# Kernel tuning notes

Hardware: AMD Instinct MI355X
Metric: run time of the kernel (lower is better)

## Reference

```python
import jax, jax.numpy as jnp
import numpy as np
import math

TOPK = 13
NUM_CLASSES = 80
ALPHA = 1.0
BETA = 6.0
EPS = 1e-9


def _ciou(box1, box2, eps=1e-7):
    # box1: (b, n, 1, 4) gt xyxy, box2: (b, 1, A, 4) pred xyxy -> (b, n, A)
    b1x1, b1y1, b1x2, b1y2 = [box1[..., i] for i in range(4)]
    b2x1, b2y1, b2x2, b2y2 = [box2[..., i] for i in range(4)]
    w1, h1 = b1x2 - b1x1, b1y2 - b1y1
    w2, h2 = b2x2 - b2x1, b2y2 - b2y1
    inter = jnp.clip(jnp.minimum(b1x2, b2x2) - jnp.maximum(b1x1, b2x1), 0.0) * \
            jnp.clip(jnp.minimum(b1y2, b2y2) - jnp.maximum(b1y1, b2y1), 0.0)
    union = w1 * h1 + w2 * h2 - inter + eps
    iou = inter / union
    cw = jnp.maximum(b1x2, b2x2) - jnp.minimum(b1x1, b2x1)
    ch = jnp.maximum(b1y2, b2y2) - jnp.minimum(b1y1, b2y1)
    c2 = cw * cw + ch * ch + eps
    rho2 = ((b2x1 + b2x2 - b1x1 - b1x2) ** 2 + (b2y1 + b2y2 - b1y1 - b1y2) ** 2) / 4.0
    v = (4.0 / math.pi ** 2) * (jnp.arctan(w2 / (h2 + eps)) - jnp.arctan(w1 / (h1 + eps))) ** 2
    alpha = jax.lax.stop_gradient(v / (v - iou + (1.0 + eps)))
    return iou - (rho2 / c2 + v * alpha)


def _assign(pd_scores, pd_bboxes, anc_points, gt_labels, gt_probs, gt_bboxes, mask_gt):
    b, A, C = pd_scores.shape
    n = gt_bboxes.shape[1]
    bidx = jnp.arange(b)
    labels = gt_labels.reshape(b, n).astype(jnp.int32)

    # --- get_box_metrics ---
    bbox_scores = pd_scores[bidx[:, None], :, labels]                      # (b, n, A)
    overlaps = jnp.clip(_ciou(gt_bboxes[:, :, None, :], pd_bboxes[:, None, :, :]), 0.0)
    align_metric = bbox_scores ** ALPHA * overlaps ** BETA                 # (b, n, A)

    # --- select_candidates_in_gts ---
    lt, rb = gt_bboxes[..., :2], gt_bboxes[..., 2:]
    deltas = jnp.concatenate([anc_points[None, None] - lt[:, :, None],
                              rb[:, :, None] - anc_points[None, None]], axis=-1)
    mask_in_gts = (deltas.min(-1) > EPS).astype(pd_scores.dtype)           # (b, n, A)

    # --- select_topk_candidates ---
    metrics = align_metric * mask_in_gts
    _, topk_idxs = jax.lax.top_k(metrics, TOPK)
    topk_mask = jnp.broadcast_to(mask_gt.astype(bool), (b, n, TOPK))
    topk_idxs = jnp.where(topk_mask, topk_idxs, 0)
    cnt = jnp.zeros((b, n, A), jnp.int32).at[
        bidx[:, None, None], jnp.arange(n)[None, :, None], topk_idxs].add(1)
    is_in_topk = jnp.where(cnt > 1, 0, cnt).astype(metrics.dtype)
    mask_pos = is_in_topk * mask_in_gts * mask_gt                          # (b, n, A)

    # --- select_highest_overlaps ---
    tgt = (jnp.arange(n)[None, :, None] * mask_pos).astype(jnp.int32)
    max_mask = overlaps == overlaps.max(axis=1, keepdims=True)
    tgt = tgt * max_mask.astype(jnp.int32)                                 # (b, n, A)
    unique_bbox_idx = tgt.argmax(1)                                        # (b, A)
    fg_mask = mask_pos.sum(-2)                                             # (b, A)

    # --- get_targets ---
    tgt_flat = tgt + (bidx * n)[:, None, None]                             # (b, n, A)
    target_labels = labels.reshape(-1)[tgt_flat]                           # (b, n, A)
    sel = jnp.take_along_axis(tgt_flat, unique_bbox_idx[:, None, :], axis=1)[:, 0]
    target_bboxes = gt_bboxes.reshape(-1, 4)[sel]                          # (b, A, 4)

    # hard targets: per-anchor class histogram over gt axis, corrected
    hard = jnp.zeros((b, A, C), jnp.int32).at[
        bidx[:, None, None], jnp.arange(A)[None, None, :], target_labels].add(1)
    fg_columns = hard.sum(1).argmax(1)                                     # (b,)
    diff = (n - fg_mask).astype(jnp.int32)                                 # (b, A)
    col_mask = jax.nn.one_hot(fg_columns, C, dtype=jnp.int32)[:, None, :]  # (b, 1, C)
    non_fg_count = (hard * (1 - col_mask)).sum(-1)                         # (b, A)
    hard = hard - diff[..., None] * col_mask
    denom = (fg_mask - non_fg_count)[..., None] * col_mask                 # (b, A, C) float
    safe = jnp.where(denom != 0, denom, 1.0)
    hard = jnp.where(denom != 0, jnp.trunc(hard / safe).astype(jnp.int32), hard)
    hard = jnp.clip(hard, 0, 1)  # multilabel (>1) clamped to 1, negatives to 0

    # --- normalization of target scores ---
    pos_align = (align_metric * mask_pos).max(-1, keepdims=True)           # (b, n, 1)
    pos_overlaps = (overlaps * mask_pos).max(-1, keepdims=True)
    norm = (align_metric * pos_overlaps * mask_pos / (pos_align + EPS)).max(-2)[..., None]  # (b, A, 1)
    target_scores = hard.astype(pd_scores.dtype) * norm                    # (b, A, C)
    return target_bboxes, target_scores, fg_mask.astype(bool), tgt


def setup_inputs() -> dict:
    key = jax.random.key(0)
    ks = jax.random.split(key, 8)
    B, N, C = 32, 32, 80
    # YOLO anchor-point grid for 640x640, strides 8/16/32 -> A = 8400
    pts = []
    for s, g in ((8, 80), (16, 40), (32, 20)):
        c = (jnp.arange(g, dtype=jnp.float32) + 0.5) * s
        yy, xx = jnp.meshgrid(c, c, indexing="ij")
        pts.append(jnp.stack([xx.ravel(), yy.ravel()], -1))
    anc_points = jnp.concatenate(pts, 0)
    A = anc_points.shape[0]
    pd_scores = jax.random.uniform(ks[0], (B, A, C), jnp.float32)
    pcxy = anc_points[None] + 20.0 * jax.random.normal(ks[1], (B, A, 2), jnp.float32)
    pwh = jax.random.uniform(ks[2], (B, A, 2), jnp.float32, minval=10.0, maxval=120.0)
    pd_bboxes = jnp.concatenate([pcxy - pwh / 2, pcxy + pwh / 2], -1)
    gcxy = jax.random.uniform(ks[3], (B, N, 2), jnp.float32, minval=60.0, maxval=580.0)
    gwh = jax.random.uniform(ks[4], (B, N, 2), jnp.float32, minval=10.0, maxval=120.0)
    gt_bboxes = jnp.concatenate([gcxy - gwh / 2, gcxy + gwh / 2], -1)
    gt_labels = jax.random.randint(ks[5], (B, N, 1), 0, C).astype(jnp.int32)
    gt_probs = jax.random.uniform(ks[6], (B, N, 1), jnp.float32)
    n_valid = jax.random.randint(ks[7], (B, 1, 1), 1, N + 1)
    mask_gt = (jnp.arange(N)[None, :, None] < n_valid).astype(jnp.float32)
    return {"pd_scores": pd_scores, "pd_bboxes": pd_bboxes, "anc_points": anc_points,
            "gt_labels": gt_labels, "gt_probs": gt_probs, "gt_bboxes": gt_bboxes,
            "mask_gt": mask_gt}


def reference(pd_scores, pd_bboxes, anc_points, gt_labels, gt_probs, gt_bboxes, mask_gt):
    return _assign(pd_scores, pd_bboxes, anc_points, gt_labels, gt_probs, gt_bboxes, mask_gt)
```

## Files before the change

kernel.cpp:

```cpp
#include <hip/hip_runtime.h>
#include <math.h>

#define BB 32
#define NN 32
#define AA 8400
#define CC 80
#define TK 13
#define CAND 512
#define MAXP (NN*TK)

__device__ int      g_ccnt[BB*NN];
__device__ int      g_cand[BB*NN*CAND];
__device__ unsigned g_posmask[BB*AA];
__device__ float    g_posalign[BB*NN];
__device__ float    g_posov[BB*NN];
__device__ int      g_pcnt[BB];
__device__ int      g_plist[BB*MAXP];

struct PdPre { float x1,y1,x2,y2, area, sx, sy, at; };

__device__ __forceinline__ float ciou_j(const PdPre& q, float4 g, float garea,
                                        float gsx, float gsy, float gatan) {
  float iw = fmaxf(fminf(q.x2, g.z) - fmaxf(q.x1, g.x), 0.0f);
  float ih = fmaxf(fminf(q.y2, g.w) - fmaxf(q.y1, g.y), 0.0f);
  float inter = iw * ih;
  float uni = q.area + garea - inter + 1e-7f;
  float iou = inter / uni;
  float cw = fmaxf(q.x2, g.z) - fminf(q.x1, g.x);
  float ch = fmaxf(q.y2, g.w) - fminf(q.y1, g.y);
  float c2 = cw*cw + ch*ch + 1e-7f;
  float dx = gsx - q.sx, dy = gsy - q.sy;
  float rho2 = (dx*dx + dy*dy) * 0.25f;
  float dat = gatan - q.at;
  float v = (float)(4.0/(M_PI*M_PI)) * dat * dat;
  float alpha = v / (v - iou + (1.0f + 1e-7f));
  return fmaxf(iou - (rho2/c2 + v*alpha), 0.0f);
}

__device__ __forceinline__ PdPre pd_prep(float4 p) {
  PdPre q;
  float w1 = p.z - p.x, h1 = p.w - p.y;
  q.x1 = p.x; q.y1 = p.y; q.x2 = p.z; q.y2 = p.w;
  q.area = w1*h1; q.sx = p.x + p.z; q.sy = p.y + p.w;
  q.at = atanf(w1 / (h1 + 1e-7f));
  return q;
}

__global__ __launch_bounds__(256) void kfill(const float* __restrict__ gt_bboxes,
                                             float* __restrict__ out_bbox,
                                             float* __restrict__ out_scores,
                                             float* __restrict__ out_fg,
                                             float* __restrict__ out_tgt) {
  const size_t NS4 = (size_t)BB*AA*CC/4;
  const size_t NT4 = (size_t)BB*NN*AA/4;
  const size_t NF4 = (size_t)BB*AA/4;
  const size_t NP4 = (size_t)BB*AA/4;
  const size_t NB4 = (size_t)BB*AA;
  const size_t total = NS4 + NT4 + NF4 + NP4 + NB4;
  float4 z4 = make_float4(0.f,0.f,0.f,0.f);
  for (size_t i = (size_t)blockIdx.x*256 + threadIdx.x; i < total;
       i += (size_t)gridDim.x*256) {
    if (i < NS4) ((float4*)out_scores)[i] = z4;
    else if (i < NS4+NT4) ((float4*)out_tgt)[i-NS4] = z4;
    else if (i < NS4+NT4+NF4) ((float4*)out_fg)[i-NS4-NT4] = z4;
    else if (i < NS4+NT4+NF4+NP4) ((float4*)g_posmask)[i-NS4-NT4-NF4] = z4;
    else {
      size_t k = i - NS4 - NT4 - NF4 - NP4;
      int b = (int)(k / AA);
      ((float4*)out_bbox)[k] = *(const float4*)&gt_bboxes[b*NN*4];
    }
  }
  size_t gid = (size_t)blockIdx.x*256 + threadIdx.x;
  if (gid < BB*NN) g_ccnt[gid] = 0;
  if (gid < BB) g_pcnt[gid] = 0;
}

__global__ __launch_bounds__(256) void kA(const float* __restrict__ anc,
                                          const float* __restrict__ gt_bboxes,
                                          const float* __restrict__ mask_gt) {
  int b = blockIdx.y, t = threadIdx.x;
  int a = blockIdx.x*256 + t;
  __shared__ __align__(16) float4 gbox[NN];
  __shared__ int smask[NN];
  if (t < NN) {
    gbox[t] = *(const float4*)&gt_bboxes[(b*NN + t)*4];
    smask[t] = (mask_gt[b*NN + t] != 0.0f) ? 1 : 0;
  }
  __syncthreads();
  if (a >= AA) return;
  float2 an = ((const float2*)anc)[a];
  #pragma unroll
  for (int j = 0; j < NN; ++j) {
    if (!smask[j]) continue;
    float4 g = gbox[j];
    float mn = fminf(fminf(an.x - g.x, an.y - g.y), fminf(g.z - an.x, g.w - an.y));
    if (mn > 1e-9f) {
      int s = atomicAdd(&g_ccnt[b*NN + j], 1);
      if (s < CAND) g_cand[(size_t)(b*NN + j)*CAND + s] = a;
    }
  }
}

__global__ __launch_bounds__(64) void k2(const float* __restrict__ mask_gt,
                                         const float* __restrict__ pd_scores,
                                         const float* __restrict__ pd_bboxes,
                                         const float* __restrict__ anc,
                                         const int* __restrict__ gt_labels,
                                         const float* __restrict__ gt_bboxes) {
  int bj = blockIdx.x;
  int b = bj >> 5, j = bj & 31;
  int lane = threadIdx.x;
  bool valid = (mask_gt[bj] != 0.0f);
  if (!valid) {
    if (lane == 0) { g_posalign[bj] = 0.0f; g_posov[bj] = 0.0f; }
    return;
  }
  int cnt = g_ccnt[bj]; if (cnt > CAND) cnt = CAND;
  int labj = gt_labels[bj];
  float4 g = *(const float4*)&gt_bboxes[bj*4];
  float w2 = g.z - g.x, h2 = g.w - g.y;
  float garea = w2*h2, gsx = g.x + g.z, gsy = g.y + g.w;
  float gatan = atanf(w2 / (h2 + 1e-7f));
  const float2* anc2 = (const float2*)anc;

  unsigned long long tk[TK];
  #pragma unroll
  for (int i = 0; i < TK; ++i) tk[i] = 0ull;
  auto ins = [&](unsigned long long key) {
    if (key > tk[TK-1]) {
      tk[TK-1] = key;
      #pragma unroll
      for (int i = TK-1; i > 0; --i) {
        if (tk[i] > tk[i-1]) {
          unsigned long long tmp = tk[i-1]; tk[i-1] = tk[i]; tk[i] = tmp;
        }
      }
    }
  };
  for (int c = lane; c < cnt; c += 64) {
    int a = g_cand[(size_t)bj*CAND + c];
    float4 p = *(const float4*)&pd_bboxes[(size_t)(b*AA + a)*4];
    float sc = pd_scores[(size_t)(b*AA + a)*CC + labj];
    PdPre q = pd_prep(p);
    float ov = ciou_j(q, g, garea, gsx, gsy, gatan);
    float ov2 = ov*ov;
    float metric = sc * (ov2*ov2*ov2);
    ins(((unsigned long long)__float_as_uint(metric) << 32)
        | (unsigned long long)(0xFFFFFFFFu - (unsigned)a));
  }
  if (lane < TK) {
    float2 an = anc2[lane];
    float mn = fminf(fminf(an.x - g.x, an.y - g.y), fminf(g.z - an.x, g.w - an.y));
    if (!(mn > 1e-9f))
      ins((unsigned long long)(0xFFFFFFFFu - (unsigned)lane));
  }
  unsigned long long myk = 0ull;
  for (int r = 0; r < TK; ++r) {
    unsigned long long m = tk[0];
    #pragma unroll
    for (int o = 32; o > 0; o >>= 1) {
      unsigned long long other = __shfl_xor(m, o, 64);
      if (other > m) m = other;
    }
    if (tk[0] == m) {
      #pragma unroll
      for (int i = 0; i < TK-1; ++i) tk[i] = tk[i+1];
      tk[TK-1] = 0ull;
    }
    if (lane == r) myk = m;
  }
  float pa = 0.0f, po = 0.0f;
  if (lane < TK && myk != 0ull) {
    unsigned a = 0xFFFFFFFFu - (unsigned)(myk & 0xFFFFFFFFull);
    float val = __uint_as_float((unsigned)(myk >> 32));
    float2 an = anc2[a];
    float mn = fminf(fminf(an.x - g.x, an.y - g.y), fminf(g.z - an.x, g.w - an.y));
    if (mn > 1e-9f) {
      unsigned old = atomicOr(&g_posmask[b*AA + a], 1u << j);
      if (old == 0u) {
        int idx = atomicAdd(&g_pcnt[b], 1);
        g_plist[b*MAXP + idx] = (int)a;
      }
      float4 p = *(const float4*)&pd_bboxes[(size_t)(b*AA + a)*4];
      PdPre q = pd_prep(p);
      float ov = ciou_j(q, g, garea, gsx, gsy, gatan);
      pa = val; po = ov;
    }
  }
  #pragma unroll
  for (int o = 32; o > 0; o >>= 1) {
    pa = fmaxf(pa, __shfl_xor(pa, o, 64));
    po = fmaxf(po, __shfl_xor(po, o, 64));
  }
  if (lane == 0) { g_posalign[bj] = pa; g_posov[bj] = po; }
}

__global__ __launch_bounds__(256) void k3(const float* __restrict__ pd_scores,
                                          const float* __restrict__ pd_bboxes,
                                          const float* __restrict__ gt_bboxes,
                                          const int* __restrict__ gt_labels,
                                          float* __restrict__ out_bbox,
                                          float* __restrict__ out_fg,
                                          float* __restrict__ out_tgt,
                                          float* __restrict__ out_scores) {
  int b = blockIdx.y, t = threadIdx.x;
  __shared__ __align__(16) float4 gbox[NN];
  __shared__ float garea[NN], gsx[NN], gsy[NN], gatan[NN], pal[NN], pov[NN];
  __shared__ int lab[NN];
  if (t < NN) {
    float4 g = *(const float4*)&gt_bboxes[(b*NN + t)*4];
    gbox[t] = g;
    float w2 = g.z - g.x, h2 = g.w - g.y;
    gsx[t] = g.x + g.z; gsy[t] = g.y + g.w;
    garea[t] = w2*h2;
    gatan[t] = atanf(w2 / (h2 + 1e-7f));
    lab[t] = gt_labels[b*NN + t];
    pal[t] = g_posalign[b*NN + t];
    pov[t] = g_posov[b*NN + t];
  }
  __syncthreads();
  int npos = g_pcnt[b];
  int si = blockIdx.x*8 + (t >> 5);
  if (si >= npos) return;
  int j = t & 31;
  int a = g_plist[b*MAXP + si];
  unsigned pm = g_posmask[b*AA + a];
  float4 p = *(const float4*)&pd_bboxes[(size_t)(b*AA + a)*4];
  PdPre q = pd_prep(p);
  float ovj = ciou_j(q, gbox[j], garea[j], gsx[j], gsy[j], gatan[j]);
  float maxo = ovj;
  #pragma unroll
  for (int o = 16; o > 0; o >>= 1) maxo = fmaxf(maxo, __shfl_xor(maxo, o, 64));
  bool pmj = (pm >> j) & 1u;
  bool tb = pmj && (ovj == maxo) && (j > 0);
  unsigned long long bal = __ballot(tb);
  unsigned tm = (t & 32) ? (unsigned)(bal >> 32) : (unsigned)(bal & 0xffffffffull);
  float contrib = 0.0f;
  if (pmj) {
    float sc = pd_scores[(size_t)(b*AA + a)*CC + lab[j]];
    float ov2 = ovj*ovj;
    float al = sc * (ov2*ov2*ov2);
    contrib = al * pov[j] / (pal[j] + 1e-9f);
  }
  float nrm = contrib;
  #pragma unroll
  for (int o = 16; o > 0; o >>= 1) nrm = fmaxf(nrm, __shfl_xor(nrm, o, 64));
  if (tb) out_tgt[(size_t)(b*NN + j)*AA + a] = (float)j;
  int fg = __popc(pm);
  int F = lab[0];
  unsigned m0 = 0u, m1 = 0u, m2 = 0u;
  int z = NN - __popc(tm);
  int cntF = z;
  {
    int l0 = lab[0];
    if (l0 < 32) m0 |= 1u << l0; else if (l0 < 64) m1 |= 1u << (l0-32); else m2 |= 1u << (l0-64);
  }
  unsigned tmp = tm;
  while (tmp) {
    int jj = __ffs(tmp) - 1; tmp &= tmp - 1;
    int l = lab[jj];
    if (l < 32) m0 |= 1u << l; else if (l < 64) m1 |= 1u << (l-32); else m2 |= 1u << (l-64);
    cntF += (l == F) ? 1 : 0;
  }
  bool hFv = (cntF + fg) != NN;
  size_t base = (size_t)(b*AA + a)*CC;
  {
    int c = j;
    bool bit = (m0 >> j) & 1u;
    bool ind = (c == F) ? hFv : bit;
    out_scores[base + c] = ind ? nrm : 0.0f;
  }
  {
    int c = j + 32;
    bool bit = (m1 >> j) & 1u;
    bool ind = (c == F) ? hFv : bit;
    out_scores[base + c] = ind ? nrm : 0.0f;
  }
  if (j < 16) {
    int c = j + 64;
    bool bit = (m2 >> j) & 1u;
    bool ind = (c == F) ? hFv : bit;
    out_scores[base + c] = ind ? nrm : 0.0f;
  }
  if (j == 0) {
    out_fg[b*AA + a] = 1.0f;
    int jmax = tm ? (31 - __clz(tm)) : 0;
    *(float4*)&out_bbox[(size_t)(b*AA + a)*4] = gbox[jmax];
  }
}

extern "C" void kernel_launch(void* const* d_in, const int* in_sizes, int n_in,
                              void* d_out, int out_size, void* d_ws, size_t ws_size,
                              hipStream_t stream) {
  const float* pd_scores = (const float*)d_in[0];
  const float* pd_bboxes = (const float*)d_in[1];
  const float* anc       = (const float*)d_in[2];
  const int*   gt_labels = (const int*)d_in[3];
  const float* gt_bboxes = (const float*)d_in[5];
  const float* mask_gt   = (const float*)d_in[6];

  float* out_bbox   = (float*)d_out;
  float* out_scores = out_bbox + (size_t)BB*AA*4;
  float* out_fg     = out_scores + (size_t)BB*AA*CC;
  float* out_tgt    = out_fg + (size_t)BB*AA;

  kfill<<<2048, 256, 0, stream>>>(gt_bboxes, out_bbox, out_scores, out_fg, out_tgt);
  dim3 ga((AA + 255)/256, BB);
  kA<<<ga, 256, 0, stream>>>(anc, gt_bboxes, mask_gt);
  k2<<<BB*NN, 64, 0, stream>>>(mask_gt, pd_scores, pd_bboxes, anc, gt_labels, gt_bboxes);
  dim3 g3((MAXP + 7)/8, BB);
  k3<<<g3, 256, 0, stream>>>(pd_scores, pd_bboxes, gt_bboxes, gt_labels,
                             out_bbox, out_fg, out_tgt, out_scores);
}
```

Baseline: 54.59 us.

## Fuse candidate gather into fill kernel and merge top-k with scatter per batch

After: 77.50 us. +42.0%, slower.

```diff
diff --git a/kernel.cpp b/kernel.cpp
--- a/kernel.cpp
+++ b/kernel.cpp
@@ -7,15 +7,11 @@
 #define CC 80
 #define TK 13
 #define CAND 512
+#define NSEG 33
 #define MAXP (NN*TK)
 
-__device__ int      g_ccnt[BB*NN];
-__device__ int      g_cand[BB*NN*CAND];
-__device__ unsigned g_posmask[BB*AA];
-__device__ float    g_posalign[BB*NN];
-__device__ float    g_posov[BB*NN];
-__device__ int      g_pcnt[BB];
-__device__ int      g_plist[BB*MAXP];
+__device__ int g_ccnt[BB*NN];
+__device__ int g_cand[BB*NN*CAND];
 
 struct PdPre { float x1,y1,x2,y2, area, sx, sy, at; };
 
@@ -46,167 +42,74 @@
   return q;
 }
 
-__global__ __launch_bounds__(256) void kfill(const float* __restrict__ gt_bboxes,
-                                             float* __restrict__ out_bbox,
-                                             float* __restrict__ out_scores,
-                                             float* __restrict__ out_fg,
-                                             float* __restrict__ out_tgt) {
+__global__ __launch_bounds__(256) void kfillA(const float* __restrict__ anc,
+                                              const float* __restrict__ gt_bboxes,
+                                              const float* __restrict__ mask_gt,
+                                              float* __restrict__ out_bbox,
+                                              float* __restrict__ out_scores,
+                                              float* __restrict__ out_fg,
+                                              float* __restrict__ out_tgt) {
+  int bx = blockIdx.x, t = threadIdx.x;
+  if (bx < NSEG*BB) {
+    int b = bx / NSEG, seg = bx % NSEG;
+    __shared__ __align__(16) float4 gbox[NN];
+    __shared__ int smask[NN];
+    if (t < NN) {
+      gbox[t] = *(const float4*)&gt_bboxes[(b*NN + t)*4];
+      smask[t] = (mask_gt[b*NN + t] != 0.0f) ? 1 : 0;
+    }
+    __syncthreads();
+    int a = seg*256 + t;
+    if (a < AA) {
+      float2 an = ((const float2*)anc)[a];
+      #pragma unroll
+      for (int j = 0; j < NN; ++j) {
+        if (!smask[j]) continue;
+        float4 g = gbox[j];
+        float mn = fminf(fminf(an.x - g.x, an.y - g.y), fminf(g.z - an.x, g.w - an.y));
+        if (mn > 1e-9f) {
+          int s = atomicAdd(&g_ccnt[b*NN + j], 1);
+          if (s < CAND) g_cand[(size_t)(b*NN + j)*CAND + s] = a;
+        }
+      }
+    }
+  }
   const size_t NS4 = (size_t)BB*AA*CC/4;
   const size_t NT4 = (size_t)BB*NN*AA/4;
   const size_t NF4 = (size_t)BB*AA/4;
-  const size_t NP4 = (size_t)BB*AA/4;
   const size_t NB4 = (size_t)BB*AA;
-  const size_t total = NS4 + NT4 + NF4 + NP4 + NB4;
+  const size_t total = NS4 + NT4 + NF4 + NB4;
   float4 z4 = make_float4(0.f,0.f,0.f,0.f);
-  for (size_t i = (size_t)blockIdx.x*256 + threadIdx.x; i < total;
-       i += (size_t)gridDim.x*256) {
+  for (size_t i = (size_t)bx*256 + t; i < total; i += (size_t)gridDim.x*256) {
     if (i < NS4) ((float4*)out_scores)[i] = z4;
     else if (i < NS4+NT4) ((float4*)out_tgt)[i-NS4] = z4;
     else if (i < NS4+NT4+NF4) ((float4*)out_fg)[i-NS4-NT4] = z4;
-    else if (i < NS4+NT4+NF4+NP4) ((float4*)g_posmask)[i-NS4-NT4-NF4] = z4;
     else {
-      size_t k = i - NS4 - NT4 - NF4 - NP4;
+      size_t k = i - NS4 - NT4 - NF4;
       int b = (int)(k / AA);
       ((float4*)out_bbox)[k] = *(const float4*)&gt_bboxes[b*NN*4];
     }
   }
-  size_t gid = (size_t)blockIdx.x*256 + threadIdx.x;
-  if (gid < BB*NN) g_ccnt[gid] = 0;
-  if (gid < BB) g_pcnt[gid] = 0;
-}
-
-__global__ __launch_bounds__(256) void kA(const float* __restrict__ anc,
-                                          const float* __restrict__ gt_bboxes,
-                                          const float* __restrict__ mask_gt) {
-  int b = blockIdx.y, t = threadIdx.x;
-  int a = blockIdx.x*256 + t;
-  __shared__ __align__(16) float4 gbox[NN];
-  __shared__ int smask[NN];
-  if (t < NN) {
-    gbox[t] = *(const float4*)&gt_bboxes[(b*NN + t)*4];
-    smask[t] = (mask_gt[b*NN + t] != 0.0f) ? 1 : 0;
-  }
-  __syncthreads();
-  if (a >= AA) return;
-  float2 an = ((const float2*)anc)[a];
-  #pragma unroll
-  for (int j = 0; j < NN; ++j) {
-    if (!smask[j]) continue;
-    float4 g = gbox[j];
-    float mn = fminf(fminf(an.x - g.x, an.y - g.y), fminf(g.z - an.x, g.w - an.y));
-    if (mn > 1e-9f) {
-      int s = atomicAdd(&g_ccnt[b*NN + j], 1);
-      if (s < CAND) g_cand[(size_t)(b*NN + j)*CAND + s] = a;
-    }
-  }
-}
-
-__global__ __launch_bounds__(64) void k2(const float* __restrict__ mask_gt,
-                                         const float* __restrict__ pd_scores,
-                                         const float* __restrict__ pd_bboxes,
-                                         const float* __restrict__ anc,
-                                         const int* __restrict__ gt_labels,
-                                         const float* __restrict__ gt_bboxes) {
-  int bj = blockIdx.x;
-  int b = bj >> 5, j = bj & 31;
-  int lane = threadIdx.x;
-  bool valid = (mask_gt[bj] != 0.0f);
-  if (!valid) {
-    if (lane == 0) { g_posalign[bj] = 0.0f; g_posov[bj] = 0.0f; }
-    return;
-  }
-  int cnt = g_ccnt[bj]; if (cnt > CAND) cnt = CAND;
-  int labj = gt_labels[bj];
-  float4 g = *(const float4*)&gt_bboxes[bj*4];
-  float w2 = g.z - g.x, h2 = g.w - g.y;
-  float garea = w2*h2, gsx = g.x + g.z, gsy = g.y + g.w;
-  float gatan = atanf(w2 / (h2 + 1e-7f));
-  const float2* anc2 = (const float2*)anc;
-
-  unsigned long long tk[TK];
-  #pragma unroll
-  for (int i = 0; i < TK; ++i) tk[i] = 0ull;
-  auto ins = [&](unsigned long long key) {
-    if (key > tk[TK-1]) {
-      tk[TK-1] = key;
-      #pragma unroll
-      for (int i = TK-1; i > 0; --i) {
-        if (tk[i] > tk[i-1]) {
-          unsigned long long tmp = tk[i-1]; tk[i-1] = tk[i]; tk[i] = tmp;
-        }
-      }
-    }
-  };
-  for (int c = lane; c < cnt; c += 64) {
-    int a = g_cand[(size_t)bj*CAND + c];
-    float4 p = *(const float4*)&pd_bboxes[(size_t)(b*AA + a)*4];
-    float sc = pd_scores[(size_t)(b*AA + a)*CC + labj];
-    PdPre q = pd_prep(p);
-    float ov = ciou_j(q, g, garea, gsx, gsy, gatan);
-    float ov2 = ov*ov;
-    float metric = sc * (ov2*ov2*ov2);
-    ins(((unsigned long long)__float_as_uint(metric) << 32)
-        | (unsigned long long)(0xFFFFFFFFu - (unsigned)a));
-  }
-  if (lane < TK) {
-    float2 an = anc2[lane];
-    float mn = fminf(fminf(an.x - g.x, an.y - g.y), fminf(g.z - an.x, g.w - an.y));
-    if (!(mn > 1e-9f))
-      ins((unsigned long long)(0xFFFFFFFFu - (unsigned)lane));
-  }
-  unsigned long long myk = 0ull;
-  for (int r = 0; r < TK; ++r) {
-    unsigned long long m = tk[0];
-    #pragma unroll
-    for (int o = 32; o > 0; o >>= 1) {
-      unsigned long long other = __shfl_xor(m, o, 64);
-      if (other > m) m = other;
-    }
-    if (tk[0] == m) {
-      #pragma unroll
-      for (int i = 0; i < TK-1; ++i) tk[i] = tk[i+1];
-      tk[TK-1] = 0ull;
-    }
-    if (lane == r) myk = m;
-  }
-  float pa = 0.0f, po = 0.0f;
-  if (lane < TK && myk != 0ull) {
-    unsigned a = 0xFFFFFFFFu - (unsigned)(myk & 0xFFFFFFFFull);
-    float val = __uint_as_float((unsigned)(myk >> 32));
-    float2 an = anc2[a];
-    float mn = fminf(fminf(an.x - g.x, an.y - g.y), fminf(g.z - an.x, g.w - an.y));
-    if (mn > 1e-9f) {
-      unsigned old = atomicOr(&g_posmask[b*AA + a], 1u << j);
-      if (old == 0u) {
-        int idx = atomicAdd(&g_pcnt[b], 1);
-        g_plist[b*MAXP + idx] = (int)a;
-      }
-      float4 p = *(const float4*)&pd_bboxes[(size_t)(b*AA + a)*4];
-      PdPre q = pd_prep(p);
-      float ov = ciou_j(q, g, garea, gsx, gsy, gatan);
-      pa = val; po = ov;
-    }
-  }
-  #pragma unroll
-  for (int o = 32; o > 0; o >>= 1) {
-    pa = fmaxf(pa, __shfl_xor(pa, o, 64));
-    po = fmaxf(po, __shfl_xor(po, o, 64));
-  }
-  if (lane == 0) { g_posalign[bj] = pa; g_posov[bj] = po; }
-}
-
-__global__ __launch_bounds__(256) void k3(const float* __restrict__ pd_scores,
-                                          const float* __restrict__ pd_bboxes,
-                                          const float* __restrict__ gt_bboxes,
-                                          const int* __restrict__ gt_labels,
-                                          float* __restrict__ out_bbox,
-                                          float* __restrict__ out_fg,
-                                          float* __restrict__ out_tgt,
-                                          float* __restrict__ out_scores) {
-  int b = blockIdx.y, t = threadIdx.x;
+}
+
+__global__ __launch_bounds__(1024) void k23(const float* __restrict__ mask_gt,
+                                            const float* __restrict__ pd_scores,
+                                            const float* __restrict__ pd_bboxes,
+                                            const float* __restrict__ anc,
+                                            const int* __restrict__ gt_labels,
+                                            const float* __restrict__ gt_bboxes,
+                                            float* __restrict__ out_bbox,
+                                            float* __restrict__ out_fg,
+                                            float* __restrict__ out_tgt,
+                                            float* __restrict__ out_scores) {
+  int b = blockIdx.x, t = threadIdx.x;
+  __shared__ unsigned s_posmask[AA];
   __shared__ __align__(16) float4 gbox[NN];
   __shared__ float garea[NN], gsx[NN], gsy[NN], gatan[NN], pal[NN], pov[NN];
   __shared__ int lab[NN];
+  __shared__ int s_pcnt;
+  __shared__ int s_plist[MAXP];
+  for (int a = t; a < AA; a += 1024) s_posmask[a] = 0u;
   if (t < NN) {
     float4 g = *(const float4*)&gt_bboxes[(b*NN + t)*4];
     gbox[t] = g;
@@ -215,77 +118,160 @@
     garea[t] = w2*h2;
     gatan[t] = atanf(w2 / (h2 + 1e-7f));
     lab[t] = gt_labels[b*NN + t];
-    pal[t] = g_posalign[b*NN + t];
-    pov[t] = g_posov[b*NN + t];
-  }
+    pal[t] = 0.0f; pov[t] = 0.0f;
+  }
+  if (t == 0) s_pcnt = 0;
   __syncthreads();
-  int npos = g_pcnt[b];
-  int si = blockIdx.x*8 + (t >> 5);
-  if (si >= npos) return;
-  int j = t & 31;
-  int a = g_plist[b*MAXP + si];
-  unsigned pm = g_posmask[b*AA + a];
-  float4 p = *(const float4*)&pd_bboxes[(size_t)(b*AA + a)*4];
-  PdPre q = pd_prep(p);
-  float ovj = ciou_j(q, gbox[j], garea[j], gsx[j], gsy[j], gatan[j]);
-  float maxo = ovj;
-  #pragma unroll
-  for (int o = 16; o > 0; o >>= 1) maxo = fmaxf(maxo, __shfl_xor(maxo, o, 64));
-  bool pmj = (pm >> j) & 1u;
-  bool tb = pmj && (ovj == maxo) && (j > 0);
-  unsigned long long bal = __ballot(tb);
-  unsigned tm = (t & 32) ? (unsigned)(bal >> 32) : (unsigned)(bal & 0xffffffffull);
-  float contrib = 0.0f;
-  if (pmj) {
-    float sc = pd_scores[(size_t)(b*AA + a)*CC + lab[j]];
-    float ov2 = ovj*ovj;
-    float al = sc * (ov2*ov2*ov2);
-    contrib = al * pov[j] / (pal[j] + 1e-9f);
-  }
-  float nrm = contrib;
-  #pragma unroll
-  for (int o = 16; o > 0; o >>= 1) nrm = fmaxf(nrm, __shfl_xor(nrm, o, 64));
-  if (tb) out_tgt[(size_t)(b*NN + j)*AA + a] = (float)j;
-  int fg = __popc(pm);
-  int F = lab[0];
-  unsigned m0 = 0u, m1 = 0u, m2 = 0u;
-  int z = NN - __popc(tm);
-  int cntF = z;
-  {
-    int l0 = lab[0];
-    if (l0 < 32) m0 |= 1u << l0; else if (l0 < 64) m1 |= 1u << (l0-32); else m2 |= 1u << (l0-64);
-  }
-  unsigned tmp = tm;
-  while (tmp) {
-    int jj = __ffs(tmp) - 1; tmp &= tmp - 1;
-    int l = lab[jj];
-    if (l < 32) m0 |= 1u << l; else if (l < 64) m1 |= 1u << (l-32); else m2 |= 1u << (l-64);
-    cntF += (l == F) ? 1 : 0;
-  }
-  bool hFv = (cntF + fg) != NN;
-  size_t base = (size_t)(b*AA + a)*CC;
-  {
-    int c = j;
-    bool bit = (m0 >> j) & 1u;
-    bool ind = (c == F) ? hFv : bit;
-    out_scores[base + c] = ind ? nrm : 0.0f;
-  }
-  {
-    int c = j + 32;
-    bool bit = (m1 >> j) & 1u;
-    bool ind = (c == F) ? hFv : bit;
-    out_scores[base + c] = ind ? nrm : 0.0f;
-  }
-  if (j < 16) {
-    int c = j + 64;
-    bool bit = (m2 >> j) & 1u;
-    bool ind = (c == F) ? hFv : bit;
-    out_scores[base + c] = ind ? nrm : 0.0f;
-  }
-  if (j == 0) {
-    out_fg[b*AA + a] = 1.0f;
-    int jmax = tm ? (31 - __clz(tm)) : 0;
-    *(float4*)&out_bbox[(size_t)(b*AA + a)*4] = gbox[jmax];
+  int w = t >> 6, lane = t & 63;
+  const float2* anc2 = (const float2*)anc;
+  for (int p = 0; p < 2; ++p) {
+    int j = (w << 1) | p;
+    bool valid = (mask_gt[b*NN + j] != 0.0f);
+    if (valid) {
+      int cnt = g_ccnt[b*NN + j]; if (cnt > CAND) cnt = CAND;
+      int labj = lab[j];
+      float4 g = gbox[j];
+      float ga = garea[j], gx = gsx[j], gy = gsy[j], gat = gatan[j];
+      unsigned long long tk[TK];
+      #pragma unroll
+      for (int i = 0; i < TK; ++i) tk[i] = 0ull;
+      auto ins = [&](unsigned long long key) {
+        if (key > tk[TK-1]) {
+          tk[TK-1] = key;
+          #pragma unroll
+          for (int i = TK-1; i > 0; --i) {
+            if (tk[i] > tk[i-1]) {
+              unsigned long long tmp = tk[i-1]; tk[i-1] = tk[i]; tk[i] = tmp;
+            }
+          }
+        }
+      };
+      for (int c = lane; c < cnt; c += 64) {
+        int a = g_cand[(size_t)(b*NN + j)*CAND + c];
+        float4 pp = *(const float4*)&pd_bboxes[(size_t)(b*AA + a)*4];
+        float sc = pd_scores[(size_t)(b*AA + a)*CC + labj];
+        PdPre q = pd_prep(pp);
+        float ov = ciou_j(q, g, ga, gx, gy, gat);
+        float ov2 = ov*ov;
+        float metric = sc * (ov2*ov2*ov2);
+        ins(((unsigned long long)__float_as_uint(metric) << 32)
+            | (unsigned long long)(0xFFFFFFFFu - (unsigned)a));
+      }
+      if (lane < TK) {
+        float2 an = anc2[lane];
+        float mn = fminf(fminf(an.x - g.x, an.y - g.y), fminf(g.z - an.x, g.w - an.y));
+        if (!(mn > 1e-9f))
+          ins((unsigned long long)(0xFFFFFFFFu - (unsigned)lane));
+      }
+      unsigned long long myk = 0ull;
+      for (int r = 0; r < TK; ++r) {
+        unsigned long long m = tk[0];
+        #pragma unroll
+        for (int o = 32; o > 0; o >>= 1) {
+          unsigned long long other = __shfl_xor(m, o, 64);
+          if (other > m) m = other;
+        }
+        if (tk[0] == m) {
+          #pragma unroll
+          for (int i = 0; i < TK-1; ++i) tk[i] = tk[i+1];
+          tk[TK-1] = 0ull;
+        }
+        if (lane == r) myk = m;
+      }
+      float pa = 0.0f, po = 0.0f;
+      if (lane < TK && myk != 0ull) {
+        unsigned a = 0xFFFFFFFFu - (unsigned)(myk & 0xFFFFFFFFull);
+        float val = __uint_as_float((unsigned)(myk >> 32));
+        float2 an = anc2[a];
+        float mn = fminf(fminf(an.x - g.x, an.y - g.y), fminf(g.z - an.x, g.w - an.y));
+        if (mn > 1e-9f) {
+          unsigned old = atomicOr(&s_posmask[a], 1u << j);
+          if (old == 0u) {
+            int idx = atomicAdd(&s_pcnt, 1);
+            s_plist[idx] = (int)a;
+          }
+          float4 pp = *(const float4*)&pd_bboxes[(size_t)(b*AA + a)*4];
+          PdPre q = pd_prep(pp);
+          float ov = ciou_j(q, g, ga, gx, gy, gat);
+          pa = val; po = ov;
+        }
+      }
+      #pragma unroll
+      for (int o = 32; o > 0; o >>= 1) {
+        pa = fmaxf(pa, __shfl_xor(pa, o, 64));
+        po = fmaxf(po, __shfl_xor(po, o, 64));
+      }
+      if (lane == 0) { pal[j] = pa; pov[j] = po; }
+    }
+  }
+  __syncthreads();
+  int npos = s_pcnt;
+  int hw = t >> 5, j = t & 31;
+  for (int si = hw; si < npos; si += 32) {
+    int a = s_plist[si];
+    unsigned pm = s_posmask[a];
+    float4 pp = *(const float4*)&pd_bboxes[(size_t)(b*AA + a)*4];
+    PdPre q = pd_prep(pp);
+    float ovj = ciou_j(q, gbox[j], garea[j], gsx[j], gsy[j], gatan[j]);
+    float maxo = ovj;
+    #pragma unroll
+    for (int o = 16; o > 0; o >>= 1) maxo = fmaxf(maxo, __shfl_xor(maxo, o, 64));
+    bool pmj = (pm >> j) & 1u;
+    bool tb = pmj && (ovj == maxo) && (j > 0);
+    unsigned long long bal = __ballot(tb);
+    unsigned tm = (t & 32) ? (unsigned)(bal >> 32) : (unsigned)(bal & 0xffffffffull);
+    float contrib = 0.0f;
+    if (pmj) {
+      float sc = pd_scores[(size_t)(b*AA + a)*CC + lab[j]];
+      float ov2 = ovj*ovj;
+      float al = sc * (ov2*ov2*ov2);
+      contrib = al * pov[j] / (pal[j] + 1e-9f);
+    }
+    float nrm = contrib;
+    #pragma unroll
+    for (int o = 16; o > 0; o >>= 1) nrm = fmaxf(nrm, __shfl_xor(nrm, o, 64));
+    if (tb) out_tgt[(size_t)(b*NN + j)*AA + a] = (float)j;
+    int fg = __popc(pm);
+    int F = lab[0];
+    unsigned m0 = 0u, m1 = 0u, m2 = 0u;
+    int z = NN - __popc(tm);
+    int cntF = z;
+    {
+      int l0 = lab[0];
+      if (l0 < 32) m0 |= 1u << l0; else if (l0 < 64) m1 |= 1u << (l0-32); else m2 |= 1u << (l0-64);
+    }
+    unsigned tmp = tm;
+    while (tmp) {
+      int jj = __ffs(tmp) - 1; tmp &= tmp - 1;
+      int l = lab[jj];
+      if (l < 32) m0 |= 1u << l; else if (l < 64) m1 |= 1u << (l-32); else m2 |= 1u << (l-64);
+      cntF += (l == F) ? 1 : 0;
+    }
+    bool hFv = (cntF + fg) != NN;
+    size_t base = (size_t)(b*AA + a)*CC;
+    {
+      int c = j;
+      bool bit = (m0 >> j) & 1u;
+      bool ind = (c == F) ? hFv : bit;
+      out_scores[base + c] = ind ? nrm : 0.0f;
+    }
+    {
+      int c = j + 32;
+      bool bit = (m1 >> j) & 1u;
+      bool ind = (c == F) ? hFv : bit;
+      out_scores[base + c] = ind ? nrm : 0.0f;
+    }
+    if (j < 16) {
+      int c = j + 64;
+      bool bit = (m2 >> j) & 1u;
+      bool ind = (c == F) ? hFv : bit;
+      out_scores[base + c] = ind ? nrm : 0.0f;
+    }
+    if (j == 0) {
+      out_fg[b*AA + a] = 1.0f;
+      int jmax = tm ? (31 - __clz(tm)) : 0;
+      *(float4*)&out_bbox[(size_t)(b*AA + a)*4] = gbox[jmax];
+    }
   }
 }
 
@@ -304,11 +290,13 @@
   float* out_fg     = out_scores + (size_t)BB*AA*CC;
   float* out_tgt    = out_fg + (size_t)BB*AA;
 
-  kfill<<<2048, 256, 0, stream>>>(gt_bboxes, out_bbox, out_scores, out_fg, out_tgt);
-  dim3 ga((AA + 255)/256, BB);
-  kA<<<ga, 256, 0, stream>>>(anc, gt_bboxes, mask_gt);
-  k2<<<BB*NN, 64, 0, stream>>>(mask_gt, pd_scores, pd_bboxes, anc, gt_labels, gt_bboxes);
-  dim3 g3((MAXP + 7)/8, BB);
-  k3<<<g3, 256, 0, stream>>>(pd_scores, pd_bboxes, gt_bboxes, gt_labels,
-                             out_bbox, out_fg, out_tgt, out_scores);
-}
+  void* ccnt_ptr = nullptr;
+  hipGetSymbolAddress(&ccnt_ptr, HIP_SYMBOL(g_ccnt));
+  hipMemsetAsync(ccnt_ptr, 0, BB*NN*sizeof(int), stream);
+
+  kfillA<<<2048, 256, 0, stream>>>(anc, gt_bboxes, mask_gt,
+                                   out_bbox, out_scores, out_fg, out_tgt);
+  k23<<<BB, 1024, 0, stream>>>(mask_gt, pd_scores, pd_bboxes, anc,
+                               gt_labels, gt_bboxes,
+                               out_bbox, out_fg, out_tgt, out_scores);
+}
```
